# Optimization experiments

Hardware: AMD Instinct MI355X
Metric: run time of the kernel (lower is better)

The kernel has to match this reference:

```python
import jax, jax.numpy as jnp
import numpy as np

# bitsandbytes NF4 codebook (16 levels)
NF4_CODE = jnp.array([
    -1.0, -0.6961928009986877, -0.5250730514526367, -0.39491748809814453,
    -0.28444138169288635, -0.18477343022823334, -0.09105003625154495, 0.0,
    0.07958029955625534, 0.16093020141124725, 0.24611230194568634,
    0.33791524171829224, 0.44070982933044434, 0.5626170039176941,
    0.7229568362236023, 1.0], dtype=jnp.float32)

L, D, KV, F, V = 2, 4096, 1024, 14336, 32000   # layers, d_model, kv_dim, ffn, vocab
H, HK, HD = 32, 8, 128                          # q heads, kv heads, head dim
B, S = 2, 1024
BLK = 64                                        # NF4 quant blocksize
ROPE_THETA = 500000.0
RMS_EPS = 1e-5


def _dequant(idx, absmax, shape):
    # idx: uint8 flat codes in [0,16); absmax: fp32 per-64-element block scale
    w = NF4_CODE[idx.astype(jnp.int32)]
    return (w.reshape(-1, BLK) * absmax[:, None]).reshape(shape)


def _rmsnorm(x, w):
    return x * jax.lax.rsqrt(jnp.mean(x * x, axis=-1, keepdims=True) + RMS_EPS) * w


def _rope(x, cos, sin):
    d2 = x.shape[-1] // 2
    x1, x2 = x[..., :d2], x[..., d2:]
    return jnp.concatenate([x1 * cos - x2 * sin, x2 * cos + x1 * sin], axis=-1)


def setup_inputs() -> dict:
    key = jax.random.key(0)
    ks = iter(jax.random.split(key, 64))

    def idx(n):
        return jax.random.randint(next(ks), (n,), 0, 16).astype(jnp.uint8)

    def amax(n):
        return jax.random.uniform(next(ks), (n // BLK,), minval=0.01, maxval=0.05)

    def qw(n):
        return (jnp.stack([idx(n) for _ in range(L)]),
                jnp.stack([amax(n) for _ in range(L)]))

    inp = {}
    inp["input_ids"] = jax.random.randint(next(ks), (B, S), 0, V, dtype=jnp.int32)
    inp["attention_mask"] = jnp.ones((B, S), dtype=jnp.int32)
    inp["embed"] = jax.random.normal(next(ks), (V, D), dtype=jnp.float32) * 0.02
    inp["q_idx"], inp["q_absmax"] = qw(D * D)
    inp["k_idx"], inp["k_absmax"] = qw(KV * D)
    inp["v_idx"], inp["v_absmax"] = qw(KV * D)
    inp["o_idx"], inp["o_absmax"] = qw(D * D)
    inp["gate_idx"], inp["gate_absmax"] = qw(F * D)
    inp["up_idx"], inp["up_absmax"] = qw(F * D)
    inp["down_idx"], inp["down_absmax"] = qw(D * F)
    inp["ln1_w"] = jnp.ones((L, D), dtype=jnp.float32)
    inp["ln2_w"] = jnp.ones((L, D), dtype=jnp.float32)
    inp["final_ln_w"] = jnp.ones((D,), dtype=jnp.float32)
    return inp


def reference(input_ids, attention_mask, embed,
              q_idx, q_absmax, k_idx, k_absmax, v_idx, v_absmax,
              o_idx, o_absmax, gate_idx, gate_absmax, up_idx, up_absmax,
              down_idx, down_absmax, ln1_w, ln2_w, final_ln_w):
    b, s = input_ids.shape
    h = embed[input_ids]                                  # [B,S,D]
    pos = jnp.arange(s, dtype=jnp.float32)
    inv = 1.0 / (ROPE_THETA ** (jnp.arange(0, HD, 2, dtype=jnp.float32) / HD))
    ang = pos[:, None] * inv[None, :]                     # [S,HD/2]
    cos = jnp.cos(ang)[None, :, None, :]
    sin = jnp.sin(ang)[None, :, None, :]
    causal = jnp.tril(jnp.ones((s, s), dtype=bool))
    mask = causal[None, None] & (attention_mask[:, None, None, :] > 0)  # [B,1,S,S]
    neg = jnp.finfo(h.dtype).min

    for l in range(L):
        x = _rmsnorm(h, ln1_w[l])
        q = x @ _dequant(q_idx[l], q_absmax[l], (D, D)).T
        k = x @ _dequant(k_idx[l], k_absmax[l], (KV, D)).T
        v = x @ _dequant(v_idx[l], v_absmax[l], (KV, D)).T
        q = _rope(q.reshape(b, s, H, HD), cos, sin)
        k = _rope(k.reshape(b, s, HK, HD), cos, sin)
        v = v.reshape(b, s, HK, HD)
        k = jnp.repeat(k, H // HK, axis=2)                # GQA expand
        v = jnp.repeat(v, H // HK, axis=2)
        scores = jnp.einsum('bqhd,bkhd->bhqk', q, k) / np.float32(np.sqrt(HD))
        scores = jnp.where(mask, scores, neg)
        attn = jax.nn.softmax(scores, axis=-1)
        ctx = jnp.einsum('bhqk,bkhd->bqhd', attn, v).reshape(b, s, D)
        h = h + ctx @ _dequant(o_idx[l], o_absmax[l], (D, D)).T
        x = _rmsnorm(h, ln2_w[l])
        g = x @ _dequant(gate_idx[l], gate_absmax[l], (F, D)).T
        u = x @ _dequant(up_idx[l], up_absmax[l], (F, D)).T
        h = h + (jax.nn.silu(g) * u) @ _dequant(down_idx[l], down_absmax[l], (D, F)).T

    h = _rmsnorm(h, final_ln_w)                           # last hidden state
    m = attention_mask.astype(h.dtype)[..., None]         # masked mean pool
    pooled = (h * m).sum(axis=1) / jnp.clip(m.sum(axis=1), 1e-9)
    return pooled
```

## Files before the change

kernel.cpp:

```cpp
#include <hip/hip_runtime.h>
#include <hip/hip_fp16.h>
#include <cstdint>
#include <cstddef>

#define B_  2
#define S_  1024
#define D_  4096
#define KV_ 1024
#define F_  14336
#define H_  32
#define HK_ 8
#define HD_ 128
#define M_  2048

typedef _Float16 f16;
typedef f16   f16x8 __attribute__((ext_vector_type(8)));
typedef f16   f16x4 __attribute__((ext_vector_type(4)));
typedef float f32x4 __attribute__((ext_vector_type(4)));

#define AS1(p) ((const __attribute__((address_space(1))) void*)(p))
#define AS3(p) ((__attribute__((address_space(3))) void*)(p))

__device__ __constant__ float NF4_C[16] = {
 -1.0f, -0.6961928009986877f, -0.5250730514526367f, -0.39491748809814453f,
 -0.28444138169288635f, -0.18477343022823334f, -0.09105003625154495f, 0.0f,
 0.07958029955625534f, 0.16093020141124725f, 0.24611230194568634f,
 0.33791524171829224f, 0.44070982933044434f, 0.5626170039176941f,
 0.7229568362236023f, 1.0f };

__global__ void k_detect(const unsigned* __restrict__ p, int* __restrict__ flag){
    if (threadIdx.x == 0){
        int u8 = 0;
        for (int i = 0; i < 256; ++i) if (p[i] >= 16u) { u8 = 1; break; }
        *flag = u8;
    }
}

__global__ __launch_bounds__(256) void k_dequant(const void* __restrict__ idxBase, size_t elemOff,
        const float* __restrict__ amax, f16* __restrict__ out, const int* __restrict__ flag)
{
    __shared__ __half2 T[3856];
    int t = threadIdx.x;
    if (t < 256){
        int b0 = t & 15, b1 = t >> 4;
        T[b0 + (b1 << 8)] = __halves2half2(__float2half(NF4_C[b0]), __float2half(NF4_C[b1]));
    }
    __syncthreads();
    size_t i = ((size_t)blockIdx.x * 256 + t) * 16;
    float am = amax[i >> 6];
    __half2 am2 = __float2half2_rn(am);
    union { __half2 h2[8]; uint4 u4[2]; } R;
    if (*flag){
        uint4 u = *(const uint4*)((const uint8_t*)idxBase + elemOff + i);
        unsigned w[4] = {u.x, u.y, u.z, u.w};
        #pragma unroll
        for (int j = 0; j < 4; ++j){
            R.h2[j*2+0] = __hmul2(T[w[j] & 0xFFFFu], am2);
            R.h2[j*2+1] = __hmul2(T[w[j] >> 16],     am2);
        }
    } else {
        const int4* s4 = (const int4*)((const int*)idxBase + elemOff + i);
        #pragma unroll
        for (int j = 0; j < 4; ++j){
            int4 a = s4[j];
            R.h2[j*2+0] = __hmul2(T[a.x | (a.y << 8)], am2);
            R.h2[j*2+1] = __hmul2(T[a.z | (a.w << 8)], am2);
        }
    }
    uint4* o = (uint4*)(out + i);
    o[0] = R.u4[0]; o[1] = R.u4[1];
}

__global__ __launch_bounds__(256) void k_embed(const int* __restrict__ ids,
        const float* __restrict__ E, float* __restrict__ Hh)
{
    int row = blockIdx.x, t = threadIdx.x;
    int id = ids[row];
    const float4* s4 = (const float4*)(E + (size_t)id * D_);
    float4* d4 = (float4*)(Hh + (size_t)row * D_);
    #pragma unroll
    for (int i = 0; i < 4; ++i) d4[t + 256*i] = s4[t + 256*i];
}

__global__ __launch_bounds__(256) void k_ropetab(float* __restrict__ cosT, float* __restrict__ sinT){
    int id = blockIdx.x * 256 + threadIdx.x;
    int d = id & 63, s = id >> 6;
    float inv = powf(500000.0f, -(float)d * (1.0f/64.0f));
    float ang = (float)s * inv;
    cosT[id] = cosf(ang);
    sinT[id] = sinf(ang);
}

template<int F16OUT>
__global__ __launch_bounds__(256) void k_rmsnorm(const float* __restrict__ X,
        const float* __restrict__ W, void* __restrict__ outv)
{
    int row = blockIdx.x, t = threadIdx.x;
    const float4* x4 = (const float4*)(X + (size_t)row * D_);
    float4 xs[4]; float ss = 0.f;
    #pragma unroll
    for (int i = 0; i < 4; ++i){
        xs[i] = x4[t + 256*i];
        ss += xs[i].x*xs[i].x + xs[i].y*xs[i].y + xs[i].z*xs[i].z + xs[i].w*xs[i].w;
    }
    for (int m = 32; m; m >>= 1) ss += __shfl_xor(ss, m, 64);
    __shared__ float red[4];
    if ((t & 63) == 0) red[t >> 6] = ss;
    __syncthreads();
    ss = red[0] + red[1] + red[2] + red[3];
    float rs = rsqrtf(ss * (1.0f / D_) + 1e-5f);
    #pragma unroll
    for (int i = 0; i < 4; ++i){
        int c0 = (t + 256*i) * 4;
        float4 wv = *(const float4*)(W + c0);
        float o0 = xs[i].x*rs*wv.x, o1 = xs[i].y*rs*wv.y;
        float o2 = xs[i].z*rs*wv.z, o3 = xs[i].w*rs*wv.w;
        if (F16OUT){
            f16x4 ov = { (f16)o0, (f16)o1, (f16)o2, (f16)o3 };
            *(f16x4*)((f16*)outv + (size_t)row * D_ + c0) = ov;
        } else {
            float4 ov = {o0, o1, o2, o3};
            *(float4*)((float*)outv + (size_t)row * D_ + c0) = ov;
        }
    }
}

template<int LNH>
__global__ __launch_bounds__(256) void k_rope(const f16* __restrict__ in, int istr,
        f16* __restrict__ outp, const float* __restrict__ cosT, const float* __restrict__ sinT)
{
    int p = blockIdx.x * 256 + threadIdx.x;
    int d = p & 63;
    int h = (p >> 6) & ((1 << LNH) - 1);
    int s = (p >> (6 + LNH)) & (S_ - 1);
    int b = p >> (16 + LNH);
    size_t ib = (size_t)(b * S_ + s) * istr + (size_t)h * HD_;
    float x1 = (float)in[ib + d], x2 = (float)in[ib + 64 + d];
    float c = cosT[s*64 + d], sn = sinT[s*64 + d];
    size_t ob = (((size_t)((b << LNH) + h)) * S_ + (size_t)s) * HD_;
    outp[ob + d]      = (f16)(x1 * c - x2 * sn);
    outp[ob + 64 + d] = (f16)(x2 * c + x1 * sn);
}

__global__ __launch_bounds__(256) void k_vtrans(const f16* __restrict__ in, int istr,
        f16* __restrict__ outp){
    int p = blockIdx.x * 256 + threadIdx.x;
    int s  = p & (S_ - 1);
    int d  = (p >> 10) & (HD_ - 1);
    int hk = (p >> 17) & (HK_ - 1);
    int b  = p >> 20;
    f16 v = in[(size_t)(b * S_ + s) * istr + (size_t)hk * HD_ + d];
    outp[(((size_t)(b * HK_ + hk)) * HD_ + d) * S_ + s] = v;
}

__global__ __launch_bounds__(256) void k_softmax(__half* __restrict__ P, const int* __restrict__ amask, int bh0){
    int rid = blockIdx.x;
    int z = rid >> 10, sq = rid & (S_ - 1);
    int b = (bh0 + z) >> 5;
    __half* row = P + (size_t)z * S_ * S_ + (size_t)sq * S_;
    int t = threadIdx.x;
    const __half2* r2 = (const __half2*)row;
    __half2 a0 = r2[t*2], a1 = r2[t*2 + 1];
    float v[4] = { __low2float(a0), __high2float(a0), __low2float(a1), __high2float(a1) };
    int c0 = t * 4;
    #pragma unroll
    for (int j = 0; j < 4; ++j){
        int col = c0 + j;
        if (col > sq || amask[b * S_ + col] == 0) v[j] = -1e30f;
    }
    float mx = fmaxf(fmaxf(v[0], v[1]), fmaxf(v[2], v[3]));
    for (int m = 32; m; m >>= 1) mx = fmaxf(mx, __shfl_xor(mx, m, 64));
    __shared__ float red[4];
    if ((t & 63) == 0) red[t >> 6] = mx;
    __syncthreads();
    mx = fmaxf(fmaxf(red[0], red[1]), fmaxf(red[2], red[3]));
    float p4[4], sum = 0.f;
    #pragma unroll
    for (int j = 0; j < 4; ++j){ p4[j] = __expf(v[j] - mx); sum += p4[j]; }
    for (int m = 32; m; m >>= 1) sum += __shfl_xor(sum, m, 64);
    __syncthreads();
    if ((t & 63) == 0) red[t >> 6] = sum;
    __syncthreads();
    sum = red[0] + red[1] + red[2] + red[3];
    float inv = 1.0f / fmaxf(sum, 1e-30f);
    __half2* w2 = (__half2*)row;
    w2[t*2]     = __floats2half2_rn(p4[0]*inv, p4[1]*inv);
    w2[t*2 + 1] = __floats2half2_rn(p4[2]*inv, p4[3]*inv);
}

template<int OUT, int BM>
__global__ __launch_bounds__(256) void k_gemm(const f16* __restrict__ A, const f16* __restrict__ Bp,
        void* __restrict__ Cv, const f16* __restrict__ G,
        int Kd, int ldc, float scale, int bh0)
{
    __shared__ f16 As[128 * 64];
    __shared__ f16 Bs[128 * 64];
    int t = threadIdx.x;
    int wave = t >> 6, lane = t & 63;
    int wr = wave >> 1, wc = wave & 1;
    int lr = lane & 15, lg = lane >> 4;
    int row0 = blockIdx.y * 128, col0 = blockIdx.x * 128;

    size_t aOff = 0, bOff = 0, cOff = 0;
    if (BM == 1){
        if (col0 > row0 + 127) return;
        int bh = bh0 + blockIdx.z;
        aOff = (size_t)bh * (S_ * HD_);
        bOff = (size_t)((bh >> 5) * HK_ + ((bh & 31) >> 2)) * (S_ * HD_);
        cOff = (size_t)blockIdx.z * (S_ * S_);
    } else if (BM == 2){
        int bh = bh0 + blockIdx.z;
        aOff = (size_t)blockIdx.z * (S_ * S_);
        bOff = (size_t)((bh >> 5) * HK_ + ((bh & 31) >> 2)) * (HD_ * S_);
        cOff = (size_t)(bh >> 5) * ((size_t)S_ * D_) + (size_t)(bh & 31) * HD_;
        Kd = row0 + 128;
    }

    f32x4 zero = {0.f, 0.f, 0.f, 0.f};
    f32x4 acc[4][4];
    #pragma unroll
    for (int m = 0; m < 4; ++m)
        #pragma unroll
        for (int n = 0; n < 4; ++n) acc[m][n] = zero;

    int srow = lane >> 3;
    int scol = (lane & 7) * 8;
    const f16* Abase = A  + aOff + (size_t)row0 * Kd;
    const f16* Bbase = Bp + bOff + (size_t)col0 * Kd;
    if (BM == 1){ Abase = A + aOff + (size_t)row0 * Kd; Bbase = Bp + bOff + (size_t)col0 * Kd; }
    if (BM == 2){ Abase = A + aOff + (size_t)row0 * S_; Bbase = Bp + bOff + (size_t)col0 * S_; }

    int lda = (BM == 2) ? S_ : Kd;
    for (int k0 = 0; k0 < Kd; k0 += 64){
        if (k0) __syncthreads();
        #pragma unroll
        for (int i = 0; i < 4; ++i){
            int chunk = wave * 4 + i;
            int r = chunk * 8 + srow;
            __builtin_amdgcn_global_load_lds(AS1(Abase + (size_t)r * lda + k0 + scol), AS3(&As[chunk * 512]), 16, 0, 0);
            __builtin_amdgcn_global_load_lds(AS1(Bbase + (size_t)r * lda + k0 + scol), AS3(&Bs[chunk * 512]), 16, 0, 0);
        }
        __syncthreads();
        #pragma unroll
        for (int kk = 0; kk < 64; kk += 32){
            f16x8 av[4], bv[4];
            #pragma unroll
            for (int m = 0; m < 4; ++m) av[m] = *(const f16x8*)&As[(wr*64 + m*16 + lr)*64 + kk + lg*8];
            #pragma unroll
            for (int n = 0; n < 4; ++n) bv[n] = *(const f16x8*)&Bs[(wc*64 + n*16 + lr)*64 + kk + lg*8];
            #pragma unroll
            for (int m = 0; m < 4; ++m)
                #pragma unroll
                for (int n = 0; n < 4; ++n)
                    acc[m][n] = __builtin_amdgcn_mfma_f32_16x16x32_f16(av[m], bv[n], acc[m][n], 0, 0, 0);
        }
    }

    #pragma unroll
    for (int m = 0; m < 4; ++m)
    #pragma unroll
    for (int n = 0; n < 4; ++n)
    #pragma unroll
    for (int r = 0; r < 4; ++r){
        int row = row0 + wr*64 + m*16 + lg*4 + r;
        int col = col0 + wc*64 + n*16 + lr;
        size_t idx = cOff + (size_t)row * ldc + col;
        float v = acc[m][n][r] * scale;
        ((f16*)Cv)[idx] = (f16)v;
    }
}

template<int OUT>
__global__ __launch_bounds__(512, 1) void k_gemm3(const f16* __restrict__ A, const f16* __restrict__ Bp,
        void* __restrict__ Cv, const f16* __restrict__ G, int Kd, int ldk, int ldc)
{
    __shared__ f16 LDS[65536];
    const int t = threadIdx.x;
    const int w = t >> 6, l = t & 63;
    const int wm = w >> 2, wn = w & 3;

    int gx = gridDim.x, gy = gridDim.y;
    int nWG = gx * gy * gridDim.z;
    int n = (blockIdx.z * gy + blockIdx.y) * gx + blockIdx.x;
    int q = nWG >> 3;
    int sw = (n & 7) * q + (n >> 3);
    int bx = sw % gx; int r1 = sw / gx; int by = r1 % gy; int bz = r1 / gy;

    const int row0 = by * 256, col0 = bx * 256;
    const size_t koff = (size_t)bz * Kd;
    const int NT = Kd >> 6;

    const int swzk = ((t & 7) ^ ((t >> 3) & 7)) * 8;
    const f16* pA[2]; const f16* pB[2];
    #pragma unroll
    for (int l2 = 0; l2 < 2; ++l2){
        pA[l2] = A  + (size_t)(row0 + l2*128 + (t >> 3)) * ldk + koff + swzk;
        int wnc = (l2*64 + (t >> 3)) >> 5;
        pB[l2] = Bp + (size_t)(col0 + wnc*64 + ((t >> 3) & 31)) * ldk + koff + swzk;
    }

    auto stA = [&](int g, int tt, int buf){
        size_t so = (size_t)tt * 64;
        #pragma unroll
        for (int l2 = 0; l2 < 2; ++l2)
            __builtin_amdgcn_global_load_lds(AS1(pA[l2] + (size_t)g*64*ldk + so),
                AS3(&LDS[buf*16384 + g*8192 + l2*4096 + w*512]), 16, 0, 0);
    };
    auto stB = [&](int g, int tt, int buf){
        size_t so = (size_t)tt * 64;
        #pragma unroll
        for (int l2 = 0; l2 < 2; ++l2)
            __builtin_amdgcn_global_load_lds(AS1(pB[l2] + (size_t)g*32*ldk + so),
                AS3(&LDS[32768 + buf*16384 + g*8192 + l2*4096 + w*512]), 16, 0, 0);
    };

    const int lrow = (l & 15) * 64;
    const int kp0 = (((l >> 4))     ^ (l & 7)) * 8;
    const int kp1 = ((4 + (l >> 4)) ^ (l & 7)) * 8;

    f16x8 aR[2][4], bR0[2][2], bR1[2][2];
    auto rdA = [&](int g, int buf){
        int base = buf*16384 + g*8192 + wm*4096 + lrow;
        #pragma unroll
        for (int mf = 0; mf < 4; ++mf){
            aR[0][mf] = *(const f16x8*)&LDS[base + mf*1024 + kp0];
            aR[1][mf] = *(const f16x8*)&LDS[base + mf*1024 + kp1];
        }
    };
    auto rdB = [&](int g, int buf, f16x8 (&bR)[2][2]){
        int base = 32768 + buf*16384 + g*8192 + wn*2048 + lrow;
        #pragma unroll
        for (int nf = 0; nf < 2; ++nf){
            bR[0][nf] = *(const f16x8*)&LDS[base + nf*1024 + kp0];
            bR[1][nf] = *(const f16x8*)&LDS[base + nf*1024 + kp1];
        }
    };

    f32x4 zero = {0.f, 0.f, 0.f, 0.f};
    f32x4 acc[8][4];
    #pragma unroll
    for (int mi = 0; mi < 8; ++mi)
        #pragma unroll
        for (int ni = 0; ni < 4; ++ni) acc[mi][ni] = zero;

    #define MMQ(qm, qn, bR) { \
        __builtin_amdgcn_s_setprio(1); \
        _Pragma("unroll") \
        for (int ks = 0; ks < 2; ++ks) \
            _Pragma("unroll") \
            for (int mf = 0; mf < 4; ++mf) \
                _Pragma("unroll") \
                for (int nf = 0; nf < 2; ++nf) \
                    acc[(qm)*4+mf][(qn)*2+nf] = __builtin_amdgcn_mfma_f32_16x16x32_f16(aR[ks][mf], bR[ks][nf], acc[(qm)*4+mf][(qn)*2+nf], 0, 0, 0); \
        __builtin_amdgcn_s_setprio(0); }
    #define LGKM0 { asm volatile("s_waitcnt lgkmcnt(0)" ::: "memory"); __builtin_amdgcn_sched_barrier(0); }
    #define VM4   { asm volatile("s_waitcnt vmcnt(4)" ::: "memory"); }
    #define BAR   __builtin_amdgcn_s_barrier()

    stA(0, 0, 0); stB(1, 0, 0); stA(1, 0, 0); stB(0, 0, 0);
    if (NT > 1){ stA(0, 1, 1); stB(1, 1, 1); }
    VM4; BAR;

    for (int tt = 0; tt < NT; tt += 2){
        int c2 = (tt + 2 < NT) ? tt + 2 : NT - 1;
        int c3 = (tt + 3 < NT) ? tt + 3 : NT - 1;
        rdA(0, 0); rdB(0, 0, bR0);
        stA(1, tt+1 < NT ? tt+1 : NT-1, 1); stB(0, tt+1 < NT ? tt+1 : NT-1, 1);
        BAR; LGKM0; MMQ(0, 0, bR0); BAR;
        rdB(1, 0, bR1);
        BAR; LGKM0; MMQ(0, 1, bR1); BAR;
        rdA(1, 0);
        stA(0, c2, 0);
        BAR; LGKM0; MMQ(1, 1, bR1); BAR;
        stB(1, c2, 0);
        BAR; MMQ(1, 0, bR0); VM4; BAR;
        rdA(0, 1); rdB(0, 1, bR0);
        stA(1, c2, 0); stB(0, c2, 0);
        BAR; LGKM0; MMQ(0, 0, bR0); BAR;
        rdB(1, 1, bR1);
        BAR; LGKM0; MMQ(0, 1, bR1); BAR;
        rdA(1, 1);
        stA(0, c3, 1);
        BAR; LGKM0; MMQ(1, 1, bR1); BAR;
        stB(1, c3, 1);
        BAR; MMQ(1, 0, bR0); VM4; BAR;
    }

    #pragma unroll
    for (int mi = 0; mi < 8; ++mi)
    #pragma unroll
    for (int ni = 0; ni < 4; ++ni)
    #pragma unroll
    for (int r = 0; r < 4; ++r){
        int row = row0 + wm*128 + mi*16 + ((l >> 4) << 2) + r;
        int col = col0 + wn*64  + ni*16 + (l & 15);
        float v = acc[mi][ni][r];
        if (OUT == 0){
            ((float*)Cv)[(size_t)bz * ((size_t)M_ * ldc) + (size_t)row * ldc + col] = v;
        } else if (OUT == 2){
            ((f16*)Cv)[(size_t)row * ldc + col] = (f16)v;
        } else {
            size_t idx = (size_t)row * ldc + col;
            float g = (float)G[idx];
            float sg = g / (1.f + __expf(-g));
            ((f16*)Cv)[idx] = (f16)(sg * v);
        }
    }
    #undef MMQ
    #undef LGKM0
    #undef VM4
    #undef BAR
}

__global__ __launch_bounds__(256) void k_comb(const float* __restrict__ p0, const float* __restrict__ p1,
        float* __restrict__ outv)
{
    size_t i = ((size_t)blockIdx.x * 256 + threadIdx.x) * 4;
    float4 a = *(const float4*)(p0 + i);
    float4 b = *(const float4*)(p1 + i);
    float4 hv = *(const float4*)(outv + i);
    hv.x += a.x + b.x; hv.y += a.y + b.y; hv.z += a.z + b.z; hv.w += a.w + b.w;
    *(float4*)(outv + i) = hv;
}

__global__ __launch_bounds__(256) void k_pool1(const float* __restrict__ Hn, const int* __restrict__ amask,
        float* __restrict__ part, float* __restrict__ cntp)
{
    int d0 = blockIdx.x * 256 + threadIdx.x;
    int b  = blockIdx.y;
    int z  = blockIdx.z;
    int s0 = z * 128;
    float s = 0.f;
    for (int i = 0; i < 128; ++i){
        int row = s0 + i;
        if (amask[b * S_ + row])
            s += Hn[((size_t)(b * S_ + row)) * D_ + d0];
    }
    part[((size_t)(z * B_ + b)) * D_ + d0] = s;
    if (blockIdx.x == 0 && threadIdx.x == 0){
        float c = 0.f;
        for (int i = 0; i < 128; ++i) c += (amask[b * S_ + s0 + i] != 0) ? 1.f : 0.f;
        cntp[z * B_ + b] = c;
    }
}
__global__ __launch_bounds__(256) void k_pool2(const float* __restrict__ part, const float* __restrict__ cntp,
        float* __restrict__ outp)
{
    int gid = blockIdx.x * 256 + threadIdx.x;
    int b = gid >> 12, d = gid & (D_ - 1);
    float s = 0.f, c = 0.f;
    #pragma unroll
    for (int z = 0; z < 8; ++z){
        s += part[((size_t)(z * B_ + b)) * D_ + d];
        c += cntp[z * B_ + b];
    }
    outp[gid] = s / fmaxf(c, 1e-9f);
}

extern "C" void kernel_launch(void* const* d_in, const int* in_sizes, int n_in,
                              void* d_out, int out_size, void* d_ws, size_t ws_size,
                              hipStream_t stream)
{
    (void)in_sizes; (void)n_in; (void)out_size; (void)ws_size;
    const int*   ids   = (const int*)  d_in[0];
    const int*   amask = (const int*)  d_in[1];
    const float* embed = (const float*)d_in[2];
    const void*  qi = d_in[3];  const float* qa = (const float*)d_in[4];
    const void*  ki = d_in[5];  const float* ka = (const float*)d_in[6];
    const void*  vi = d_in[7];  const float* va = (const float*)d_in[8];
    const void*  oi = d_in[9];  const float* oa = (const float*)d_in[10];
    const void*  gi = d_in[11]; const float* ga = (const float*)d_in[12];
    const void*  ui = d_in[13]; const float* ua = (const float*)d_in[14];
    const void*  di = d_in[15]; const float* da = (const float*)d_in[16];
    const float* ln1 = (const float*)d_in[17];
    const float* ln2 = (const float*)d_in[18];
    const float* lnf = (const float*)d_in[19];

    const size_t DD  = (size_t)D_ * D_;
    const size_t KVD = (size_t)KV_ * D_;
    const size_t FD  = (size_t)F_ * D_;

    char* ws = (char*)d_ws;
    int*   flag = (int*)ws;
    float* h    = (float*)(ws + 256);
    float* cosT = (float*)(ws + 256 + 33554432);
    float* sinT = cosT + 65536;
    f16*   xin  = (f16*)(ws + 34078976);
    f16*   wbuf = (f16*)(ws + 50856192);
    char*  R4   = ws + 168296704;
    f16* qkv16 = (f16*)(R4);
    f16* qr  = (f16*)(R4 + 25165824);
    f16* kr  = (f16*)(R4 + 41943040);
    f16* vtr = (f16*)(R4 + 46137344);
    f16* ctx = (f16*)(R4 + 50331648);
    char* R5 = R4 + 67108864;
    __half* scores = (__half*)R5;
    f16*    gbuf   = (f16*)R5;
    float*  pR5_0  = (float*)R5;
    float*  pR5_1  = (float*)(R5 + 33554432);
    float*  pR4_0  = (float*)R4;
    float*  pR4_1  = (float*)(R4 + 33554432);
    float*  hn     = (float*)R4;
    float*  part   = (float*)R5;
    float*  cntp   = (float*)(R5 + 1048576);

    const float ISQ = 0.08838834764831845f;
    const int QKV_N = D_ + 2 * KV_;

    k_detect <<<1, 64, 0, stream>>>((const unsigned*)qi, flag);
    k_embed  <<<M_, 256, 0, stream>>>(ids, embed, h);
    k_ropetab<<<256, 256, 0, stream>>>(cosT, sinT);

    for (int l = 0; l < 2; ++l){
        size_t oDD = (size_t)l * DD, oKVD = (size_t)l * KVD, oFD = (size_t)l * FD;
        k_rmsnorm<1><<<M_, 256, 0, stream>>>(h, ln1 + l * D_, xin);

        k_dequant<<<DD / 4096, 256, 0, stream>>>(qi, oDD, qa + oDD/64, wbuf, flag);
        k_dequant<<<KVD / 4096, 256, 0, stream>>>(ki, oKVD, ka + oKVD/64, wbuf + DD, flag);
        k_dequant<<<KVD / 4096, 256, 0, stream>>>(vi, oKVD, va + oKVD/64, wbuf + DD + KVD, flag);
        k_gemm3<2><<<dim3(QKV_N/256, M_/256, 1), 512, 0, stream>>>(xin, wbuf, qkv16, nullptr, D_, D_, QKV_N);

        k_rope<5><<<(B_*S_*H_*64)/256, 256, 0, stream>>>(qkv16, QKV_N, qr, cosT, sinT);
        k_rope<3><<<(B_*S_*HK_*64)/256, 256, 0, stream>>>(qkv16 + D_, QKV_N, kr, cosT, sinT);
        k_vtrans <<<(B_*HK_*HD_*S_)/256, 256, 0, stream>>>(qkv16 + D_ + KV_, QKV_N, vtr);

        for (int c = 0; c < 2; ++c){
            k_gemm<2,1><<<dim3(S_/128, S_/128, 32), 256, 0, stream>>>(qr, kr, (void*)scores, nullptr, HD_, S_, ISQ, c*32);
            k_softmax<<<32 * S_, 256, 0, stream>>>(scores, amask, c*32);
            k_gemm<2,2><<<dim3(1, S_/128, 32), 256, 0, stream>>>((const f16*)scores, vtr, ctx, nullptr, S_, D_, 1.0f, c*32);
        }

        k_dequant<<<DD / 4096, 256, 0, stream>>>(oi, oDD, oa + oDD/64, wbuf, flag);
        k_gemm3<0><<<dim3(D_/256, M_/256, 2), 512, 0, stream>>>(ctx, wbuf, pR5_0, nullptr, D_/2, D_, D_);
        k_comb<<<(M_*D_)/1024, 256, 0, stream>>>(pR5_0, pR5_1, h);

        k_rmsnorm<1><<<M_, 256, 0, stream>>>(h, ln2 + l * D_, xin);
        k_dequant<<<FD / 4096, 256, 0, stream>>>(gi, oFD, ga + oFD/64, wbuf, flag);
        k_gemm3<2><<<dim3(F_/256, M_/256, 1), 512, 0, stream>>>(xin, wbuf, gbuf, nullptr, D_, D_, F_);
        k_dequant<<<FD / 4096, 256, 0, stream>>>(ui, oFD, ua + oFD/64, wbuf, flag);
        k_gemm3<3><<<dim3(F_/256, M_/256, 1), 512, 0, stream>>>(xin, wbuf, gbuf, gbuf, D_, D_, F_);
        k_dequant<<<FD / 4096, 256, 0, stream>>>(di, oFD, da + oFD/64, wbuf, flag);
        k_gemm3<0><<<dim3(D_/256, M_/256, 2), 512, 0, stream>>>(gbuf, wbuf, pR4_0, nullptr, F_/2, F_, D_);
        k_comb<<<(M_*D_)/1024, 256, 0, stream>>>(pR4_0, pR4_1, h);
    }

    k_rmsnorm<0><<<M_, 256, 0, stream>>>(h, lnf, hn);
    k_pool1<<<dim3(D_/256, B_, 8), 256, 0, stream>>>(hn, amask, part, cntp);
    k_pool2<<<(B_*D_)/256, 256, 0, stream>>>(part, cntp, (float*)d_out);
}
```

Before: 2.663 ms.

## Replace materialized attention scores with fused causal flash-attention kernel

Replaces the QK^T GEMM, separate softmax, and PV GEMM (run per half of heads with an fp16 score buffer) with one flash-attention kernel using online softmax in registers and causal tile skipping. An additive padding mask is precomputed once. This removes writing and re-reading large score matrices and several launches. In exchange, each block loops serially over key tiles with syncs and no load/compute overlap, and causal work is imbalanced across blocks.

After: 2.520 ms. 1.06x faster.

```diff
diff --git a/kernel.cpp b/kernel.cpp
--- a/kernel.cpp
+++ b/kernel.cpp
@@ -89,6 +89,11 @@
     float ang = (float)s * inv;
     cosT[id] = cosf(ang);
     sinT[id] = sinf(ang);
+}
+
+__global__ void k_maskadd(const int* __restrict__ am, float* __restrict__ ma){
+    int i = blockIdx.x * 256 + threadIdx.x;
+    ma[i] = am[i] ? 0.f : -1e30f;
 }
 
 template<int F16OUT>
@@ -153,120 +158,172 @@
     outp[(((size_t)(b * HK_ + hk)) * HD_ + d) * S_ + s] = v;
 }
 
-__global__ __launch_bounds__(256) void k_softmax(__half* __restrict__ P, const int* __restrict__ amask, int bh0){
-    int rid = blockIdx.x;
-    int z = rid >> 10, sq = rid & (S_ - 1);
-    int b = (bh0 + z) >> 5;
-    __half* row = P + (size_t)z * S_ * S_ + (size_t)sq * S_;
-    int t = threadIdx.x;
-    const __half2* r2 = (const __half2*)row;
-    __half2 a0 = r2[t*2], a1 = r2[t*2 + 1];
-    float v[4] = { __low2float(a0), __high2float(a0), __low2float(a1), __high2float(a1) };
-    int c0 = t * 4;
-    #pragma unroll
-    for (int j = 0; j < 4; ++j){
-        int col = c0 + j;
-        if (col > sq || amask[b * S_ + col] == 0) v[j] = -1e30f;
-    }
-    float mx = fmaxf(fmaxf(v[0], v[1]), fmaxf(v[2], v[3]));
-    for (int m = 32; m; m >>= 1) mx = fmaxf(mx, __shfl_xor(mx, m, 64));
-    __shared__ float red[4];
-    if ((t & 63) == 0) red[t >> 6] = mx;
+__global__ __launch_bounds__(256) void k_flash(const f16* __restrict__ Qr, const f16* __restrict__ Kr,
+        const f16* __restrict__ Vt, const float* __restrict__ mAddG, f16* __restrict__ ctx)
+{
+    __shared__ f16 KS[8192];
+    __shared__ f16 VS[8192];
+    __shared__ f16 PS[8192];
+    const int t = threadIdx.x;
+    const int w = t >> 6, l = t & 63;
+    const int lr = l & 15, lg = l >> 4;
+    const int qt = blockIdx.x, bh = blockIdx.y;
+    const int b = bh >> 5, hh = bh & 31, hk = hh >> 2;
+    const f16* Qb = Qr + ((size_t)bh * S_ + (size_t)qt*128) * HD_;
+    const f16* Kb = Kr + (size_t)(b * HK_ + hk) * S_ * HD_;
+    const f16* Vb = Vt + (size_t)(b * HK_ + hk) * HD_ * S_;
+
+    auto stage16x128 = [&](const f16* src, int lds_, f16* dst){
+        int rowl = t >> 4;
+        int cs = ((t & 15) ^ (rowl & 7)) << 3;
+        #pragma unroll
+        for (int g = 0; g < 4; ++g)
+            __builtin_amdgcn_global_load_lds(AS1(src + (size_t)(g*16 + rowl)*lds_ + cs),
+                AS3(dst + g*2048 + w*512), 16, 0, 0);
+    };
+    auto stage32x64 = [&](const f16* src, int lds_, f16* dst){
+        int rowl = t >> 3;
+        int cs = ((t & 7) ^ (rowl & 7)) << 3;
+        #pragma unroll
+        for (int g = 0; g < 4; ++g)
+            __builtin_amdgcn_global_load_lds(AS1(src + (size_t)(g*32 + rowl)*lds_ + cs),
+                AS3(dst + g*2048 + w*512), 16, 0, 0);
+    };
+
+    stage16x128(Qb, HD_, KS);
+    stage16x128(Qb + 64*HD_, HD_, VS);
     __syncthreads();
-    mx = fmaxf(fmaxf(red[0], red[1]), fmaxf(red[2], red[3]));
-    float p4[4], sum = 0.f;
-    #pragma unroll
-    for (int j = 0; j < 4; ++j){ p4[j] = __expf(v[j] - mx); sum += p4[j]; }
-    for (int m = 32; m; m >>= 1) sum += __shfl_xor(sum, m, 64);
+    f16x8 qF[2][4];
+    {
+        const f16* qsrc = (w < 2) ? KS : VS;
+        int rbase = (w & 1) * 32;
+        #pragma unroll
+        for (int m = 0; m < 2; ++m)
+            #pragma unroll
+            for (int kd = 0; kd < 4; ++kd){
+                int row = rbase + m*16 + lr;
+                qF[m][kd] = *(const f16x8*)&qsrc[row*128 + (((kd*4 + lg) ^ (row & 7)) << 3)];
+            }
+    }
     __syncthreads();
-    if ((t & 63) == 0) red[t >> 6] = sum;
-    __syncthreads();
-    sum = red[0] + red[1] + red[2] + red[3];
-    float inv = 1.0f / fmaxf(sum, 1e-30f);
-    __half2* w2 = (__half2*)row;
-    w2[t*2]     = __floats2half2_rn(p4[0]*inv, p4[1]*inv);
-    w2[t*2 + 1] = __floats2half2_rn(p4[2]*inv, p4[3]*inv);
-}
-
-template<int OUT, int BM>
-__global__ __launch_bounds__(256) void k_gemm(const f16* __restrict__ A, const f16* __restrict__ Bp,
-        void* __restrict__ Cv, const f16* __restrict__ G,
-        int Kd, int ldc, float scale, int bh0)
-{
-    __shared__ f16 As[128 * 64];
-    __shared__ f16 Bs[128 * 64];
-    int t = threadIdx.x;
-    int wave = t >> 6, lane = t & 63;
-    int wr = wave >> 1, wc = wave & 1;
-    int lr = lane & 15, lg = lane >> 4;
-    int row0 = blockIdx.y * 128, col0 = blockIdx.x * 128;
-
-    size_t aOff = 0, bOff = 0, cOff = 0;
-    if (BM == 1){
-        if (col0 > row0 + 127) return;
-        int bh = bh0 + blockIdx.z;
-        aOff = (size_t)bh * (S_ * HD_);
-        bOff = (size_t)((bh >> 5) * HK_ + ((bh & 31) >> 2)) * (S_ * HD_);
-        cOff = (size_t)blockIdx.z * (S_ * S_);
-    } else if (BM == 2){
-        int bh = bh0 + blockIdx.z;
-        aOff = (size_t)blockIdx.z * (S_ * S_);
-        bOff = (size_t)((bh >> 5) * HK_ + ((bh & 31) >> 2)) * (HD_ * S_);
-        cOff = (size_t)(bh >> 5) * ((size_t)S_ * D_) + (size_t)(bh & 31) * HD_;
-        Kd = row0 + 128;
-    }
-
-    f32x4 zero = {0.f, 0.f, 0.f, 0.f};
-    f32x4 acc[4][4];
-    #pragma unroll
-    for (int m = 0; m < 4; ++m)
-        #pragma unroll
-        for (int n = 0; n < 4; ++n) acc[m][n] = zero;
-
-    int srow = lane >> 3;
-    int scol = (lane & 7) * 8;
-    const f16* Abase = A  + aOff + (size_t)row0 * Kd;
-    const f16* Bbase = Bp + bOff + (size_t)col0 * Kd;
-    if (BM == 1){ Abase = A + aOff + (size_t)row0 * Kd; Bbase = Bp + bOff + (size_t)col0 * Kd; }
-    if (BM == 2){ Abase = A + aOff + (size_t)row0 * S_; Bbase = Bp + bOff + (size_t)col0 * S_; }
-
-    int lda = (BM == 2) ? S_ : Kd;
-    for (int k0 = 0; k0 < Kd; k0 += 64){
-        if (k0) __syncthreads();
-        #pragma unroll
-        for (int i = 0; i < 4; ++i){
-            int chunk = wave * 4 + i;
-            int r = chunk * 8 + srow;
-            __builtin_amdgcn_global_load_lds(AS1(Abase + (size_t)r * lda + k0 + scol), AS3(&As[chunk * 512]), 16, 0, 0);
-            __builtin_amdgcn_global_load_lds(AS1(Bbase + (size_t)r * lda + k0 + scol), AS3(&Bs[chunk * 512]), 16, 0, 0);
-        }
+
+    float mrow[2][4], lrow[2][4];
+    f32x4 oacc[2][8];
+    #pragma unroll
+    for (int m = 0; m < 2; ++m)
+        #pragma unroll
+        for (int r = 0; r < 4; ++r){ mrow[m][r] = -1e30f; lrow[m][r] = 0.f; }
+    #pragma unroll
+    for (int m = 0; m < 2; ++m)
+        #pragma unroll
+        for (int dn = 0; dn < 8; ++dn){ f32x4 z = {0,0,0,0}; oacc[m][dn] = z; }
+
+    const float ISQ = 0.08838834764831845f;
+    const int ktMax = 2*qt + 1;
+
+    for (int kt = 0; kt <= ktMax; ++kt){
+        stage16x128(Kb + (size_t)(kt*64)*HD_, HD_, KS);
         __syncthreads();
-        #pragma unroll
-        for (int kk = 0; kk < 64; kk += 32){
-            f16x8 av[4], bv[4];
-            #pragma unroll
-            for (int m = 0; m < 4; ++m) av[m] = *(const f16x8*)&As[(wr*64 + m*16 + lr)*64 + kk + lg*8];
-            #pragma unroll
-            for (int n = 0; n < 4; ++n) bv[n] = *(const f16x8*)&Bs[(wc*64 + n*16 + lr)*64 + kk + lg*8];
-            #pragma unroll
-            for (int m = 0; m < 4; ++m)
+
+        f32x4 sacc[2][4];
+        #pragma unroll
+        for (int m = 0; m < 2; ++m)
+            #pragma unroll
+            for (int n = 0; n < 4; ++n){ f32x4 z = {0,0,0,0}; sacc[m][n] = z; }
+        #pragma unroll
+        for (int n = 0; n < 4; ++n){
+            int krow = n*16 + lr;
+            #pragma unroll
+            for (int kd = 0; kd < 4; ++kd){
+                f16x8 kF = *(const f16x8*)&KS[krow*128 + (((kd*4 + lg) ^ (krow & 7)) << 3)];
                 #pragma unroll
-                for (int n = 0; n < 4; ++n)
-                    acc[m][n] = __builtin_amdgcn_mfma_f32_16x16x32_f16(av[m], bv[n], acc[m][n], 0, 0, 0);
-        }
-    }
-
-    #pragma unroll
-    for (int m = 0; m < 4; ++m)
-    #pragma unroll
-    for (int n = 0; n < 4; ++n)
+                for (int m = 0; m < 2; ++m)
+                    sacc[m][n] = __builtin_amdgcn_mfma_f32_16x16x32_f16(qF[m][kd], kF, sacc[m][n], 0, 0, 0);
+            }
+        }
+
+        stage32x64(Vb + kt*64, S_, VS);
+
+        float mAdd[4];
+        #pragma unroll
+        for (int n = 0; n < 4; ++n) mAdd[n] = mAddG[b*S_ + kt*64 + n*16 + lr];
+        int diag = (kt >= 2*qt);
+        #pragma unroll
+        for (int m = 0; m < 2; ++m)
+        #pragma unroll
+        for (int n = 0; n < 4; ++n)
+        #pragma unroll
+        for (int r = 0; r < 4; ++r){
+            float s = sacc[m][n][r] * ISQ + mAdd[n];
+            if (diag && (kt*64 + n*16 + lr) > (qt*128 + w*32 + m*16 + lg*4 + r)) s = -1e30f;
+            sacc[m][n][r] = s;
+        }
+        #pragma unroll
+        for (int m = 0; m < 2; ++m)
+        #pragma unroll
+        for (int r = 0; r < 4; ++r){
+            float tm = fmaxf(fmaxf(sacc[m][0][r], sacc[m][1][r]), fmaxf(sacc[m][2][r], sacc[m][3][r]));
+            #pragma unroll
+            for (int msk = 1; msk < 16; msk <<= 1) tm = fmaxf(tm, __shfl_xor(tm, msk, 64));
+            float mn = fmaxf(mrow[m][r], tm);
+            float scl = __expf(mrow[m][r] - mn);
+            mrow[m][r] = mn;
+            float rs = 0.f;
+            #pragma unroll
+            for (int n = 0; n < 4; ++n){
+                float p = __expf(sacc[m][n][r] - mn);
+                sacc[m][n][r] = p; rs += p;
+            }
+            #pragma unroll
+            for (int msk = 1; msk < 16; msk <<= 1) rs += __shfl_xor(rs, msk, 64);
+            lrow[m][r] = lrow[m][r] * scl + rs;
+            #pragma unroll
+            for (int dn = 0; dn < 8; ++dn) oacc[m][dn][r] *= scl;
+        }
+        #pragma unroll
+        for (int m = 0; m < 2; ++m)
+        #pragma unroll
+        for (int n = 0; n < 4; ++n)
+        #pragma unroll
+        for (int r = 0; r < 4; ++r){
+            int rowl = m*16 + lg*4 + r;
+            int slot = (n*2 + (lr >> 3)) ^ (rowl & 7);
+            PS[w*2048 + rowl*64 + slot*8 + (lr & 7)] = (f16)sacc[m][n][r];
+        }
+        __syncthreads();
+
+        f16x8 pF[2][2];
+        #pragma unroll
+        for (int m = 0; m < 2; ++m)
+            #pragma unroll
+            for (int kd = 0; kd < 2; ++kd){
+                int prow = m*16 + lr;
+                pF[m][kd] = *(const f16x8*)&PS[w*2048 + prow*64 + (((kd*4 + lg) ^ (prow & 7)) << 3)];
+            }
+        #pragma unroll
+        for (int dn = 0; dn < 8; ++dn){
+            int vrow = dn*16 + lr;
+            #pragma unroll
+            for (int kd = 0; kd < 2; ++kd){
+                f16x8 vF = *(const f16x8*)&VS[vrow*64 + (((kd*4 + lg) ^ (vrow & 7)) << 3)];
+                #pragma unroll
+                for (int m = 0; m < 2; ++m)
+                    oacc[m][dn] = __builtin_amdgcn_mfma_f32_16x16x32_f16(pF[m][kd], vF, oacc[m][dn], 0, 0, 0);
+            }
+        }
+        __syncthreads();
+    }
+
+    #pragma unroll
+    for (int m = 0; m < 2; ++m)
+    #pragma unroll
+    for (int dn = 0; dn < 8; ++dn)
     #pragma unroll
     for (int r = 0; r < 4; ++r){
-        int row = row0 + wr*64 + m*16 + lg*4 + r;
-        int col = col0 + wc*64 + n*16 + lr;
-        size_t idx = cOff + (size_t)row * ldc + col;
-        float v = acc[m][n][r] * scale;
-        ((f16*)Cv)[idx] = (f16)v;
+        int grow = qt*128 + w*32 + m*16 + lg*4 + r;
+        int gcol = hh*128 + dn*16 + lr;
+        float v = oacc[m][dn][r] / fmaxf(lrow[m][r], 1e-30f);
+        ctx[((size_t)(b * S_) + grow) * D_ + gcol] = (f16)v;
     }
 }
 
@@ -494,7 +551,6 @@
     f16* vtr = (f16*)(R4 + 46137344);
     f16* ctx = (f16*)(R4 + 50331648);
     char* R5 = R4 + 67108864;
-    __half* scores = (__half*)R5;
     f16*    gbuf   = (f16*)R5;
     float*  pR5_0  = (float*)R5;
     float*  pR5_1  = (float*)(R5 + 33554432);
@@ -503,13 +559,14 @@
     float*  hn     = (float*)R4;
     float*  part   = (float*)R5;
     float*  cntp   = (float*)(R5 + 1048576);
-
-    const float ISQ = 0.08838834764831845f;
+    float*  maskAdd= (float*)(ws + 310378496);
+
     const int QKV_N = D_ + 2 * KV_;
 
     k_detect <<<1, 64, 0, stream>>>((const unsigned*)qi, flag);
     k_embed  <<<M_, 256, 0, stream>>>(ids, embed, h);
     k_ropetab<<<256, 256, 0, stream>>>(cosT, sinT);
+    k_maskadd<<<(B_*S_)/256, 256, 0, stream>>>(amask, maskAdd);
 
     for (int l = 0; l < 2; ++l){
         size_t oDD = (size_t)l * DD, oKVD = (size_t)l * KVD, oFD = (size_t)l * FD;
@@ -524,11 +581,7 @@
         k_rope<3><<<(B_*S_*HK_*64)/256, 256, 0, stream>>>(qkv16 + D_, QKV_N, kr, cosT, sinT);
         k_vtrans <<<(B_*HK_*HD_*S_)/256, 256, 0, stream>>>(qkv16 + D_ + KV_, QKV_N, vtr);
 
-        for (int c = 0; c < 2; ++c){
-            k_gemm<2,1><<<dim3(S_/128, S_/128, 32), 256, 0, stream>>>(qr, kr, (void*)scores, nullptr, HD_, S_, ISQ, c*32);
-            k_softmax<<<32 * S_, 256, 0, stream>>>(scores, amask, c*32);
-            k_gemm<2,2><<<dim3(1, S_/128, 32), 256, 0, stream>>>((const f16*)scores, vtr, ctx, nullptr, S_, D_, 1.0f, c*32);
-        }
+        k_flash<<<dim3(S_/128, B_*H_), 256, 0, stream>>>(qr, kr, vtr, maskAdd, ctx);
 
         k_dequant<<<DD / 4096, 256, 0, stream>>>(oi, oDD, oa + oDD/64, wbuf, flag);
         k_gemm3<0><<<dim3(D_/256, M_/256, 2), 512, 0, stream>>>(ctx, wbuf, pR5_0, nullptr, D_/2, D_, D_);
```
